# Kernel optimization log

Measured on AMD Instinct MI355X. Metric: run time of the kernel, lower is better.

## Reference

```python
import jax, jax.numpy as jnp
import numpy as np

VOCAB = 32000
EMBED = 128
HIDDEN = 2048
LAYERS = 3
BATCH = 16


def setup_inputs() -> dict:
    key = jax.random.key(0)
    ks = jax.random.split(key, 4 + 4 * LAYERS)
    inp = {}
    inp["tokens"] = jax.random.randint(ks[0], (1, BATCH), 0, VOCAB, dtype=jnp.int64)
    inp["hidden"] = jax.random.normal(ks[1], (LAYERS, BATCH, HIDDEN), dtype=jnp.float32)
    s_e = 1.0 / np.sqrt(EMBED)
    s_h = 1.0 / np.sqrt(HIDDEN)
    inp["emb"] = jax.random.normal(ks[2], (VOCAB, EMBED), dtype=jnp.float32) * s_e
    for l in range(LAYERS):
        in_dim = EMBED if l == 0 else HIDDEN
        k0, k1, k2, k3 = jax.random.split(ks[4 + l], 4)
        inp[f"W_ih{l}"] = jax.random.normal(k0, (3 * HIDDEN, in_dim), dtype=jnp.float32) * s_h
        inp[f"W_hh{l}"] = jax.random.normal(k1, (3 * HIDDEN, HIDDEN), dtype=jnp.float32) * s_h
        inp[f"b_ih{l}"] = jax.random.normal(k2, (3 * HIDDEN,), dtype=jnp.float32) * s_h
        inp[f"b_hh{l}"] = jax.random.normal(k3, (3 * HIDDEN,), dtype=jnp.float32) * s_h
    inp["W_out"] = jax.random.normal(ks[3], (VOCAB, HIDDEN), dtype=jnp.float32) * s_h
    inp["b_out"] = jnp.zeros((VOCAB,), dtype=jnp.float32)
    return inp


def _gru_cell(x, h, W_ih, W_hh, b_ih, b_hh):
    # PyTorch GRU gate math; x: (B, in), h: (B, H)
    gi = x @ W_ih.T + b_ih  # (B, 3H)
    gh = h @ W_hh.T + b_hh  # (B, 3H)
    i_r, i_z, i_n = jnp.split(gi, 3, axis=-1)
    h_r, h_z, h_n = jnp.split(gh, 3, axis=-1)
    r = jax.nn.sigmoid(i_r + h_r)
    z = jax.nn.sigmoid(i_z + h_z)
    n = jnp.tanh(i_n + r * h_n)
    return (1.0 - z) * n + z * h


def reference(tokens, hidden, emb,
              W_ih0, W_hh0, b_ih0, b_hh0,
              W_ih1, W_hh1, b_ih1, b_hh1,
              W_ih2, W_hh2, b_ih2, b_hh2,
              W_out, b_out):
    # embedding + ReLU; tokens: (1, B) -> x: (B, E) (seq_len = 1)
    x = jax.nn.relu(emb[tokens[0]])
    Ws = [(W_ih0, W_hh0, b_ih0, b_hh0),
          (W_ih1, W_hh1, b_ih1, b_hh1),
          (W_ih2, W_hh2, b_ih2, b_hh2)]
    new_h = []
    inp = x
    for l, (Wih, Whh, bih, bhh) in enumerate(Ws):
        h_l = _gru_cell(inp, hidden[l], Wih, Whh, bih, bhh)
        new_h.append(h_l)
        inp = h_l  # top-layer output feeds next layer
    new_hidden = jnp.stack(new_h, axis=0)  # (L, B, H)
    logits = inp @ W_out.T + b_out  # (B, V)
    logp = jax.nn.log_softmax(logits, axis=1)
    return logp, new_hidden
```

## Files before the change

### kernel.cpp

```cpp
#include <hip/hip_runtime.h>
#include <cmath>


#define BB 16
#define HH 2048
#define EE 128
#define VV 32000
#define G3H (3 * HH)

__device__ __forceinline__ void fma4(float& a, const float4 w, const float4 x) {
  a = fmaf(w.x, x.x, a); a = fmaf(w.y, x.y, a);
  a = fmaf(w.z, x.z, a); a = fmaf(w.w, x.w, a);
}

__device__ __forceinline__ float foldpair(float a, float b, int m, int lane) {
  float t = (lane & m) ? a : b;
  t = __shfl_xor(t, m, 64);
  return ((lane & m) ? b : a) + t;
}

__device__ __forceinline__ float sel16(const float a[16], int i) {
  float s0 = (i & 1) ? a[1]  : a[0];
  float s1 = (i & 1) ? a[3]  : a[2];
  float s2 = (i & 1) ? a[5]  : a[4];
  float s3 = (i & 1) ? a[7]  : a[6];
  float s4 = (i & 1) ? a[9]  : a[8];
  float s5 = (i & 1) ? a[11] : a[10];
  float s6 = (i & 1) ? a[13] : a[12];
  float s7 = (i & 1) ? a[15] : a[14];
  float t0 = (i & 2) ? s1 : s0;
  float t1 = (i & 2) ? s3 : s2;
  float t2 = (i & 2) ? s5 : s4;
  float t3 = (i & 2) ? s7 : s6;
  float u0 = (i & 4) ? t1 : t0;
  float u1 = (i & 4) ? t3 : t2;
  return (i & 8) ? u1 : u0;
}

template<bool BIAS>
__device__ __forceinline__
void gemv8x8(const float* __restrict__ x, const float* __restrict__ W,
             const float* __restrict__ bias, float* __restrict__ dst,
             int ldd, int row0, int half, int lane)
{
  float acc[64];
  #pragma unroll
  for (int i = 0; i < 64; ++i) acc[i] = 0.f;

  const int kb = lane * 4;
  const float* xb = x + (size_t)half * 8 * HH;

  #pragma unroll 1
  for (int it = 0; it < 8; ++it) {
    const int k = it * 256 + kb;
    float4 xv[8];
    #pragma unroll
    for (int b = 0; b < 8; ++b)
      xv[b] = *(const float4*)(xb + b * HH + k);
    #pragma unroll
    for (int r = 0; r < 8; ++r) {
      const float4 wv = *(const float4*)(W + (size_t)(row0 + r) * HH + k);
      #pragma unroll
      for (int b = 0; b < 8; ++b) fma4(acc[r * 8 + b], wv, xv[b]);
    }
  }

  #pragma unroll
  for (int j = 0; j < 32; ++j) acc[j] = foldpair(acc[j], acc[j + 32], 1, lane);
  #pragma unroll
  for (int j = 0; j < 16; ++j) acc[j] = foldpair(acc[j], acc[j + 16], 2, lane);
  #pragma unroll
  for (int j = 0; j < 8; ++j)  acc[j] = foldpair(acc[j], acc[j + 8], 4, lane);
  #pragma unroll
  for (int j = 0; j < 4; ++j)  acc[j] = foldpair(acc[j], acc[j + 4], 8, lane);
  #pragma unroll
  for (int j = 0; j < 2; ++j)  acc[j] = foldpair(acc[j], acc[j + 2], 16, lane);
  acc[0] = foldpair(acc[0], acc[1], 32, lane);

  const int idx = ((lane & 1) << 5) | ((lane & 2) << 3) | ((lane & 4) << 1)
                | ((lane & 8) >> 1) | ((lane & 16) >> 3) | ((lane & 32) >> 5);
  const int r = idx >> 3;
  const int b = idx & 7;
  float o = acc[0];
  if (BIAS) o += bias[row0 + r];
  dst[(size_t)(half * 8 + b) * ldd + row0 + r] = o;
}

__global__ __launch_bounds__(256, 2)
void gru_l0(const float* __restrict__ emb, const int* __restrict__ tokens,
            const float* __restrict__ hprev,
            const float* __restrict__ Wih0, const float* __restrict__ Whh0,
            float* __restrict__ gi, float* __restrict__ gh)
{
  const int tid  = threadIdx.x;
  const int lane = tid & 63;
  const int wv   = tid >> 6;
  const int bx   = blockIdx.x;

  if (bx < 128) {
    const int kk = lane & 15;
    const int rg = lane >> 4;
    const int u  = bx * 4 + wv;
    const int row0 = u * 12 + rg * 3;
    float acc[3][16];
    #pragma unroll
    for (int r = 0; r < 3; ++r)
      #pragma unroll
      for (int b = 0; b < 16; ++b) acc[r][b] = 0.f;

    #pragma unroll
    for (int it = 0; it < 2; ++it) {
      const int k = it * 64 + kk * 4;
      const float4 w0 = *(const float4*)(Wih0 + (size_t)row0 * EE + k);
      const float4 w1 = *(const float4*)(Wih0 + (size_t)(row0 + 1) * EE + k);
      const float4 w2 = *(const float4*)(Wih0 + (size_t)(row0 + 2) * EE + k);
      #pragma unroll
      for (int b = 0; b < 16; ++b) {
        float4 xv = *(const float4*)(emb + (size_t)tokens[b] * EE + k);
        xv.x = fmaxf(xv.x, 0.f); xv.y = fmaxf(xv.y, 0.f);
        xv.z = fmaxf(xv.z, 0.f); xv.w = fmaxf(xv.w, 0.f);
        fma4(acc[0][b], w0, xv);
        fma4(acc[1][b], w1, xv);
        fma4(acc[2][b], w2, xv);
      }
    }
    #pragma unroll
    for (int r = 0; r < 3; ++r) {
      #pragma unroll
      for (int b = 0; b < 16; ++b) {
        float a = acc[r][b];
        a += __shfl_xor(a, 1, 64);
        a += __shfl_xor(a, 2, 64);
        a += __shfl_xor(a, 4, 64);
        a += __shfl_xor(a, 8, 64);
        acc[r][b] = a;
      }
    }
    #pragma unroll
    for (int r = 0; r < 3; ++r)
      gi[(size_t)kk * G3H + row0 + r] = sel16(acc[r], kk);
  } else {
    const int w = (bx - 128) * 4 + wv;
    gemv8x8<false>(hprev, Whh0, nullptr, gh, G3H, (w >> 1) * 8, w & 1, lane);
  }
}

__global__ __launch_bounds__(256, 2)
void gru_l12(const float* __restrict__ xprev, const float* __restrict__ hl,
             const float* __restrict__ Wih, const float* __restrict__ Whh,
             float* __restrict__ gi, float* __restrict__ gh)
{
  const int lane = threadIdx.x & 63;
  const int w = blockIdx.x * 4 + (threadIdx.x >> 6);
  if (w < 1536) {
    gemv8x8<false>(xprev, Wih, nullptr, gi, G3H, (w >> 1) * 8, w & 1, lane);
  } else {
    const int u = w - 1536;
    gemv8x8<false>(hl, Whh, nullptr, gh, G3H, (u >> 1) * 8, u & 1, lane);
  }
}

__global__ __launch_bounds__(256)
void gru_epi(const float* __restrict__ gi, const float* __restrict__ gh,
             const float* __restrict__ bih, const float* __restrict__ bhh,
             const float* __restrict__ hprev, float* __restrict__ hout)
{
  const int idx = blockIdx.x * 256 + threadIdx.x;
  const int j = idx & (HH - 1);
  const size_t base = (size_t)(idx >> 11) * G3H;
  const float ir  = gi[base + j]          + bih[j];
  const float iz  = gi[base + HH + j]     + bih[HH + j];
  const float in_ = gi[base + 2 * HH + j] + bih[2 * HH + j];
  const float hr  = gh[base + j]          + bhh[j];
  const float hz  = gh[base + HH + j]     + bhh[HH + j];
  const float hn  = gh[base + 2 * HH + j] + bhh[2 * HH + j];
  const float r = 1.f / (1.f + expf(-(ir + hr)));
  const float z = 1.f / (1.f + expf(-(iz + hz)));
  const float n = tanhf(in_ + r * hn);
  hout[idx] = (1.f - z) * n + z * hprev[idx];
}

__global__ __launch_bounds__(256, 2)
void out_kernel(const float* __restrict__ h2, const float* __restrict__ Wout,
                const float* __restrict__ bout, float* __restrict__ logits)
{
  const int lane = threadIdx.x & 63;
  const int w = blockIdx.x * 4 + (threadIdx.x >> 6);
  gemv8x8<true>(h2, Wout, bout, logits, VV, (w >> 1) * 8, w & 1, lane);
}

__global__ __launch_bounds__(1024)
void lsm_kernel(float* __restrict__ logp)
{
  const int b   = blockIdx.x;
  const int tid = threadIdx.x;
  float* row = logp + (size_t)b * VV;
  const float4* r4 = (const float4*)row;
  __shared__ float red[16];
  const int wv = tid >> 6, ln = tid & 63;

  float m = -3.4e38f;
  for (int i = tid; i < VV / 4; i += 1024) {
    float4 v = r4[i];
    m = fmaxf(m, fmaxf(fmaxf(v.x, v.y), fmaxf(v.z, v.w)));
  }
  #pragma unroll
  for (int s = 1; s < 64; s <<= 1) m = fmaxf(m, __shfl_xor(m, s, 64));
  if (ln == 0) red[wv] = m;
  __syncthreads();
  if (tid == 0) {
    float mm = red[0];
    for (int w = 1; w < 16; ++w) mm = fmaxf(mm, red[w]);
    red[0] = mm;
  }
  __syncthreads();
  const float M = red[0];
  __syncthreads();

  float s = 0.f;
  for (int i = tid; i < VV / 4; i += 1024) {
    float4 v = r4[i];
    s += expf(v.x - M) + expf(v.y - M) + expf(v.z - M) + expf(v.w - M);
  }
  #pragma unroll
  for (int t = 1; t < 64; t <<= 1) s += __shfl_xor(s, t, 64);
  if (ln == 0) red[wv] = s;
  __syncthreads();
  if (tid == 0) {
    float ss = 0.f;
    for (int w = 0; w < 16; ++w) ss += red[w];
    red[0] = M + logf(ss);
  }
  __syncthreads();
  const float L = red[0];

  float4* w4 = (float4*)row;
  for (int i = tid; i < VV / 4; i += 1024) {
    float4 v = r4[i];
    v.x -= L; v.y -= L; v.z -= L; v.w -= L;
    w4[i] = v;
  }
}

extern "C" void kernel_launch(void* const* d_in, const int* in_sizes, int n_in,
                              void* d_out, int out_size, void* d_ws, size_t ws_size,
                              hipStream_t stream)
{
  const int*   tokens = (const int*)d_in[0];
  const float* hidden = (const float*)d_in[1];
  const float* emb    = (const float*)d_in[2];
  const float* Wih0 = (const float*)d_in[3];
  const float* Whh0 = (const float*)d_in[4];
  const float* bih0 = (const float*)d_in[5];
  const float* bhh0 = (const float*)d_in[6];
  const float* Wih1 = (const float*)d_in[7];
  const float* Whh1 = (const float*)d_in[8];
  const float* bih1 = (const float*)d_in[9];
  const float* bhh1 = (const float*)d_in[10];
  const float* Wih2 = (const float*)d_in[11];
  const float* Whh2 = (const float*)d_in[12];
  const float* bih2 = (const float*)d_in[13];
  const float* bhh2 = (const float*)d_in[14];
  const float* Wout = (const float*)d_in[15];
  const float* bout = (const float*)d_in[16];

  float* outp = (float*)d_out;
  float* logp = outp;
  float* hnew = outp + (size_t)BB * VV;
  float* h0 = hnew;
  float* h1 = hnew + BB * HH;
  float* h2 = hnew + 2 * BB * HH;

  float* gi = (float*)d_ws;
  float* gh = gi + (size_t)BB * G3H;

  gru_l0<<<512, 256, 0, stream>>>(emb, tokens, hidden, Wih0, Whh0, gi, gh);
  gru_epi<<<128, 256, 0, stream>>>(gi, gh, bih0, bhh0, hidden, h0);
  gru_l12<<<768, 256, 0, stream>>>(h0, hidden + BB * HH, Wih1, Whh1, gi, gh);
  gru_epi<<<128, 256, 0, stream>>>(gi, gh, bih1, bhh1, hidden + BB * HH, h1);
  gru_l12<<<768, 256, 0, stream>>>(h1, hidden + 2 * BB * HH, Wih2, Whh2, gi, gh);
  gru_epi<<<128, 256, 0, stream>>>(gi, gh, bih2, bhh2, hidden + 2 * BB * HH, h2);
  out_kernel<<<2000, 256, 0, stream>>>(h2, Wout, bout, logp);
  lsm_kernel<<<16, 1024, 0, stream>>>(logp);
}
```

Baseline: 197.6 us.

## Split GEMV tiles into 8 rows x 4 batch per wave, sharing weights across block waves

Each wave now computes 8 weight rows against 4 batch vectors instead of 8 rows against 8, and the four waves of a block share the same 8 rows, each taking a different batch group. All 8 weight rows are loaded up front each iteration, and the accumulator count drops from 64 to 32 with a shorter shuffle reduction. The intent is to cut register pressure and raise memory-level parallelism and occupancy, with same-row weight reads across waves served from cache. In exchange the grids double and half the lanes sit idle during the final store.

Result: slower. 217.0 us (+9.8%).

```diff
diff --git a/kernel.cpp b/kernel.cpp
--- a/kernel.cpp
+++ b/kernel.cpp
@@ -39,51 +39,55 @@
 
 template<bool BIAS>
 __device__ __forceinline__
-void gemv8x8(const float* __restrict__ x, const float* __restrict__ W,
-             const float* __restrict__ bias, float* __restrict__ dst,
-             int ldd, int row0, int half, int lane)
-{
-  float acc[64];
-  #pragma unroll
-  for (int i = 0; i < 64; ++i) acc[i] = 0.f;
+void gemv8r4b(const float* __restrict__ x, const float* __restrict__ W,
+              const float* __restrict__ bias, float* __restrict__ dst,
+              int ldd, int row0, int bgrp, int lane)
+{
+  float acc[32];
+  #pragma unroll
+  for (int i = 0; i < 32; ++i) acc[i] = 0.f;
 
   const int kb = lane * 4;
-  const float* xb = x + (size_t)half * 8 * HH;
+  const float* xb = x + (size_t)bgrp * 4 * HH + kb;
+  const float* Wr = W + (size_t)row0 * HH + kb;
 
   #pragma unroll 1
   for (int it = 0; it < 8; ++it) {
-    const int k = it * 256 + kb;
-    float4 xv[8];
-    #pragma unroll
-    for (int b = 0; b < 8; ++b)
+    const int k = it * 256;
+    float4 wv[8];
+    #pragma unroll
+    for (int r = 0; r < 8; ++r)
+      wv[r] = *(const float4*)(Wr + (size_t)r * HH + k);
+    float4 xv[4];
+    #pragma unroll
+    for (int b = 0; b < 4; ++b)
       xv[b] = *(const float4*)(xb + b * HH + k);
     #pragma unroll
-    for (int r = 0; r < 8; ++r) {
-      const float4 wv = *(const float4*)(W + (size_t)(row0 + r) * HH + k);
-      #pragma unroll
-      for (int b = 0; b < 8; ++b) fma4(acc[r * 8 + b], wv, xv[b]);
-    }
-  }
-
-  #pragma unroll
-  for (int j = 0; j < 32; ++j) acc[j] = foldpair(acc[j], acc[j + 32], 1, lane);
-  #pragma unroll
-  for (int j = 0; j < 16; ++j) acc[j] = foldpair(acc[j], acc[j + 16], 2, lane);
-  #pragma unroll
-  for (int j = 0; j < 8; ++j)  acc[j] = foldpair(acc[j], acc[j + 8], 4, lane);
-  #pragma unroll
-  for (int j = 0; j < 4; ++j)  acc[j] = foldpair(acc[j], acc[j + 4], 8, lane);
-  #pragma unroll
-  for (int j = 0; j < 2; ++j)  acc[j] = foldpair(acc[j], acc[j + 2], 16, lane);
-  acc[0] = foldpair(acc[0], acc[1], 32, lane);
-
-  const int idx = ((lane & 1) << 5) | ((lane & 2) << 3) | ((lane & 4) << 1)
-                | ((lane & 8) >> 1) | ((lane & 16) >> 3) | ((lane & 32) >> 5);
-  const int r = idx >> 3;
-  const int b = idx & 7;
-  float o = acc[0];
-  if (BIAS) o += bias[row0 + r];
-  dst[(size_t)(half * 8 + b) * ldd + row0 + r] = o;
+    for (int r = 0; r < 8; ++r)
+      #pragma unroll
+      for (int b = 0; b < 4; ++b) fma4(acc[r * 4 + b], wv[r], xv[b]);
+  }
+
+  #pragma unroll
+  for (int j = 0; j < 16; ++j) acc[j] = foldpair(acc[j], acc[j + 16], 1, lane);
+  #pragma unroll
+  for (int j = 0; j < 8; ++j)  acc[j] = foldpair(acc[j], acc[j + 8], 2, lane);
+  #pragma unroll
+  for (int j = 0; j < 4; ++j)  acc[j] = foldpair(acc[j], acc[j + 4], 4, lane);
+  #pragma unroll
+  for (int j = 0; j < 2; ++j)  acc[j] = foldpair(acc[j], acc[j + 2], 8, lane);
+  acc[0] = foldpair(acc[0], acc[1], 16, lane);
+  acc[0] += __shfl_xor(acc[0], 32, 64);
+
+  const int idx = ((lane & 1) << 4) | ((lane & 2) << 2) | (lane & 4)
+                | ((lane & 8) >> 2) | ((lane & 16) >> 4);
+  const int r = idx >> 2;
+  const int b = idx & 3;
+  if (lane < 32) {
+    float o = acc[0];
+    if (BIAS) o += bias[row0 + r];
+    dst[(size_t)(bgrp * 4 + b) * ldd + row0 + r] = o;
+  }
 }
 
 __global__ __launch_bounds__(256, 2)
@@ -140,8 +144,8 @@
     for (int r = 0; r < 3; ++r)
       gi[(size_t)kk * G3H + row0 + r] = sel16(acc[r], kk);
   } else {
-    const int w = (bx - 128) * 4 + wv;
-    gemv8x8<false>(hprev, Whh0, nullptr, gh, G3H, (w >> 1) * 8, w & 1, lane);
+    const int u = bx - 128;
+    gemv8r4b<false>(hprev, Whh0, nullptr, gh, G3H, u * 8, wv, lane);
   }
 }
 
@@ -151,13 +155,10 @@
              float* __restrict__ gi, float* __restrict__ gh)
 {
   const int lane = threadIdx.x & 63;
-  const int w = blockIdx.x * 4 + (threadIdx.x >> 6);
-  if (w < 1536) {
-    gemv8x8<false>(xprev, Wih, nullptr, gi, G3H, (w >> 1) * 8, w & 1, lane);
-  } else {
-    const int u = w - 1536;
-    gemv8x8<false>(hl, Whh, nullptr, gh, G3H, (u >> 1) * 8, u & 1, lane);
-  }
+  const int wv   = threadIdx.x >> 6;
+  const int bx   = blockIdx.x;
+  if (bx < 768) gemv8r4b<false>(xprev, Wih, nullptr, gi, G3H, bx * 8, wv, lane);
+  else          gemv8r4b<false>(hl, Whh, nullptr, gh, G3H, (bx - 768) * 8, wv, lane);
 }
 
 __global__ __launch_bounds__(256)
@@ -185,8 +186,8 @@
                 const float* __restrict__ bout, float* __restrict__ logits)
 {
   const int lane = threadIdx.x & 63;
-  const int w = blockIdx.x * 4 + (threadIdx.x >> 6);
-  gemv8x8<true>(h2, Wout, bout, logits, VV, (w >> 1) * 8, w & 1, lane);
+  const int wv   = threadIdx.x >> 6;
+  gemv8r4b<true>(h2, Wout, bout, logits, VV, blockIdx.x * 8, wv, lane);
 }
 
 __global__ __launch_bounds__(1024)
@@ -274,12 +275,12 @@
   float* gi = (float*)d_ws;
   float* gh = gi + (size_t)BB * G3H;
 
-  gru_l0<<<512, 256, 0, stream>>>(emb, tokens, hidden, Wih0, Whh0, gi, gh);
+  gru_l0<<<896, 256, 0, stream>>>(emb, tokens, hidden, Wih0, Whh0, gi, gh);
   gru_epi<<<128, 256, 0, stream>>>(gi, gh, bih0, bhh0, hidden, h0);
-  gru_l12<<<768, 256, 0, stream>>>(h0, hidden + BB * HH, Wih1, Whh1, gi, gh);
+  gru_l12<<<1536, 256, 0, stream>>>(h0, hidden + BB * HH, Wih1, Whh1, gi, gh);
   gru_epi<<<128, 256, 0, stream>>>(gi, gh, bih1, bhh1, hidden + BB * HH, h1);
-  gru_l12<<<768, 256, 0, stream>>>(h1, hidden + 2 * BB * HH, Wih2, Whh2, gi, gh);
+  gru_l12<<<1536, 256, 0, stream>>>(h1, hidden + 2 * BB * HH, Wih2, Whh2, gi, gh);
   gru_epi<<<128, 256, 0, stream>>>(gi, gh, bih2, bhh2, hidden + 2 * BB * HH, h2);
-  out_kernel<<<2000, 256, 0, stream>>>(h2, Wout, bout, logp);
+  out_kernel<<<4000, 256, 0, stream>>>(h2, Wout, bout, logp);
   lsm_kernel<<<16, 1024, 0, stream>>>(logp);
 }
```
